# Optimization experiments

Measured on AMD Instinct MI355X. Metric: run time of the kernel, lower is better.

The kernel has to match this reference:

```python
import jax, jax.numpy as jnp
import numpy as np

N = 100000        # nodes
E = 1600000       # edges (avg degree 16)
IN, HID, OUT = 128, 128, 40
K = 3             # Chebyshev order
NUM_HID = 5       # hidden ChebConv layers between first and last


def setup_inputs() -> dict:
    key = jax.random.key(0)
    ks = jax.random.split(key, 8)
    s = 0.05
    return dict(
        features=jax.random.normal(ks[0], (N, IN), jnp.float32),
        src=jax.random.randint(ks[1], (E,), 0, N),
        dst=jax.random.randint(ks[2], (E,), 0, N),
        W0=jax.random.normal(ks[3], (K * IN, HID), jnp.float32) * s,
        b0=jnp.zeros((HID,), jnp.float32),
        Wh=jax.random.normal(ks[4], (NUM_HID, K * HID, HID), jnp.float32) * s,
        bh=jnp.zeros((NUM_HID, HID), jnp.float32),
        Wl=jax.random.normal(ks[5], (K * HID, OUT), jnp.float32) * s,
        bl=jnp.zeros((OUT,), jnp.float32),
    )


def _cheb_conv(X, src, dst, dinv, W, b):
    """One DGL ChebConv with lambda_max=2 (re_norm=1): relu(cat(X_0..X_{K-1}) @ W + b)."""
    def spmm(Y):  # A_hat @ Y = D^-1/2 A D^-1/2 Y via gather/segment-sum
        msg = (Y * dinv)[src]                                  # [E, d]
        return jax.ops.segment_sum(msg, dst, num_segments=N) * dinv

    X0 = X
    bases = [X0]
    X1 = -spmm(X0)                       # X_1 = -A_hat X  (re_norm - 1 == 0)
    bases.append(X1)
    for _ in range(2, K):
        X2 = -2.0 * spmm(X1) - X0        # X_t = -2 A_hat X_{t-1} - X_{t-2}
        bases.append(X2)
        X0, X1 = X1, X2
    Xt = jnp.concatenate(bases, axis=1)  # [N, K*d]
    return jax.nn.relu(Xt @ W + b)


def reference(features, src, dst, W0, b0, Wh, bh, Wl, bl):
    # symmetric normalization from in-degrees (clamped at 1), as in DGL ChebConv
    deg = jax.ops.segment_sum(jnp.ones((E,), jnp.float32), dst, num_segments=N)
    dinv = jnp.clip(deg, 1.0, None) ** -0.5
    dinv = dinv[:, None]                 # [N, 1]

    h = _cheb_conv(features, src, dst, dinv, W0, b0)
    for i in range(NUM_HID):             # dropout is identity in eval mode
        h = _cheb_conv(h, src, dst, dinv, Wh[i], bh[i])
    return _cheb_conv(h, src, dst, dinv, Wl, bl)
```

## Files before the change

kernel.cpp:

```cpp
#include <hip/hip_runtime.h>
#include <hip/hip_bf16.h>


#define NN 100000
#define EE 1600000
#define FF 128
#define NBK 1563
#define EPB 4096
#define CAP 3072
#define QTH1 25000
#define QTH2 50000
#define QTH3 75000

typedef __attribute__((ext_vector_type(8))) short short8_t;
typedef __attribute__((ext_vector_type(8))) _Float16 half8_t;
typedef __attribute__((ext_vector_type(4))) _Float16 half4_t;
typedef __attribute__((ext_vector_type(4))) float floatx4;
typedef __attribute__((ext_vector_type(4))) float accfrag;


__global__ __launch_bounds__(256) void bhist_kernel(const int* __restrict__ dst,
                                                    int* __restrict__ bcnt) {
    __shared__ int lh[NBK];
    int tid = threadIdx.x;
    for (int j = tid; j < NBK; j += 256) lh[j] = 0;
    __syncthreads();
    int e0 = blockIdx.x * EPB;
#pragma unroll
    for (int k = 0; k < EPB / 256; ++k) {
        int i = e0 + k * 256 + tid;
        if (i < EE) atomicAdd(&lh[dst[i] >> 6], 1);
    }
    __syncthreads();
    for (int j = tid; j < NBK; j += 256)
        if (lh[j] > 0) atomicAdd(&bcnt[j], lh[j]);
}

__global__ __launch_bounds__(256) void scan_p1_kernel(const int* __restrict__ cnt,
                                                      int* __restrict__ bsum, int n) {
    __shared__ int red[8];
    int i = blockIdx.x * 256 + threadIdx.x;
    int v = (i < n) ? cnt[i] : 0;
    for (int off = 32; off > 0; off >>= 1) v += __shfl_down(v, off, 64);
    int wv = threadIdx.x >> 6;
    if ((threadIdx.x & 63) == 0) red[wv] = v;
    __syncthreads();
    if (threadIdx.x == 0) bsum[blockIdx.x] = red[0] + red[1] + red[2] + red[3];
}

__global__ __launch_bounds__(1024) void scan_p2_kernel(int* __restrict__ bsum, int nb) {
    __shared__ int s[1024];
    int tid = threadIdx.x;
    int v = (tid < nb) ? bsum[tid] : 0;
    s[tid] = v;
    __syncthreads();
    for (int off = 1; off < 1024; off <<= 1) {
        int u = (tid >= off) ? s[tid - off] : 0;
        __syncthreads();
        s[tid] += u;
        __syncthreads();
    }
    if (tid < nb) bsum[tid] = s[tid] - v;
}

__global__ __launch_bounds__(256) void scan_p3_kernel(const int* __restrict__ cnt,
                                                      const int* __restrict__ bsum,
                                                      int* __restrict__ out_ptr, int n) {
    __shared__ int s[256];
    int tid = threadIdx.x;
    int i = blockIdx.x * 256 + tid;
    int v = (i < n) ? cnt[i] : 0;
    s[tid] = v;
    __syncthreads();
    for (int off = 1; off < 256; off <<= 1) {
        int u = (tid >= off) ? s[tid - off] : 0;
        __syncthreads();
        s[tid] += u;
        __syncthreads();
    }
    if (i < n) {
        int excl = bsum[blockIdx.x] + s[tid] - v;
        out_ptr[i] = excl;
        if (i == n - 1) out_ptr[n] = excl + v;
    }
}

__global__ __launch_bounds__(256) void bscatter_kernel(
    const int* __restrict__ src, const int* __restrict__ dst,
    const int* __restrict__ bptr, int* __restrict__ bfill, int* __restrict__ ebuf) {
    __shared__ int lh[NBK];
    __shared__ int lbase[NBK];
    int tid = threadIdx.x;
    for (int j = tid; j < NBK; j += 256) lh[j] = 0;
    __syncthreads();
    int e0 = blockIdx.x * EPB;
#pragma unroll
    for (int k = 0; k < EPB / 256; ++k) {
        int i = e0 + k * 256 + tid;
        if (i < EE) atomicAdd(&lh[dst[i] >> 6], 1);
    }
    __syncthreads();
    for (int j = tid; j < NBK; j += 256)
        if (lh[j] > 0) lbase[j] = atomicAdd(&bfill[j], lh[j]);
    __syncthreads();
    for (int j = tid; j < NBK; j += 256) lh[j] = 0;
    __syncthreads();
#pragma unroll
    for (int k = 0; k < EPB / 256; ++k) {
        int i = e0 + k * 256 + tid;
        if (i < EE) {
            int d = dst[i];
            int b = d >> 6;
            int off = atomicAdd(&lh[b], 1);
            ebuf[bptr[b] + lbase[b] + off] = (src[i] << 6) | (d & 63);
        }
    }
}

__global__ __launch_bounds__(256) void csr_build_kernel(
    const int* __restrict__ ebuf, const int* __restrict__ bptr,
    int* __restrict__ rowptr, int* __restrict__ colsrc,
    float* __restrict__ dinv, float* __restrict__ dinv2, float* __restrict__ sdeg) {
    __shared__ int pk[CAP];
    __shared__ int ob[CAP];
    __shared__ int cnt[256];
    __shared__ int sexcl[256];
    __shared__ int fill[256];

    int tid = threadIdx.x;
    int b = blockIdx.x;
    int start = bptr[b];
    int cb = bptr[b + 1] - start;
    if (cb > CAP) cb = CAP;

    cnt[tid] = 0; fill[tid] = 0;
    __syncthreads();

    for (int i = tid; i < cb; i += 256) {
        int v = ebuf[start + i];
        pk[i] = v;
        int srcn = v >> 6;
        int qt = (srcn >= QTH3) ? 3 : (srcn >= QTH2) ? 2 : (srcn >= QTH1) ? 1 : 0;
        atomicAdd(&cnt[((v & 63) << 2) | qt], 1);
    }
    __syncthreads();

    if (tid < 64) {
        int base = tid << 2;
        int c0 = cnt[base], c1 = cnt[base + 1], c2 = cnt[base + 2], c3 = cnt[base + 3];
        int lsum = c0 + c1 + c2 + c3;
        int inc = lsum;
        for (int off = 1; off < 64; off <<= 1) {
            int u = __shfl_up(inc, off, 64);
            if (tid >= off) inc += u;
        }
        int lex = inc - lsum;
        sexcl[base]     = lex;
        sexcl[base + 1] = lex + c0;
        sexcl[base + 2] = lex + c0 + c1;
        sexcl[base + 3] = lex + c0 + c1 + c2;
        int gnode = b * 64 + tid;
        if (gnode < NN) {
            rowptr[gnode] = start + lex;
            int d = lsum < 1 ? 1 : lsum;
            float fd = (float)d;
            dinv[gnode]  = 1.0f / sqrtf(fd);
            dinv2[gnode] = 1.0f / fd;
            sdeg[gnode]  = sqrtf(fd);
        }
    }
    if (b == 0 && tid == 0) rowptr[NN] = EE;
    __syncthreads();

    for (int i = tid; i < cb; i += 256) {
        int v = pk[i];
        int srcn = v >> 6;
        int qt = (srcn >= QTH3) ? 3 : (srcn >= QTH2) ? 2 : (srcn >= QTH1) ? 1 : 0;
        int bin = ((v & 63) << 2) | qt;
        int off = atomicAdd(&fill[bin], 1);
        ob[sexcl[bin] + off] = srcn;
    }
    __syncthreads();

    for (int i = tid; i < cb; i += 256) colsrc[start + i] = ob[i];
}


__global__ __launch_bounds__(256) void wprep_kernel(
    const float* __restrict__ W0, const float* __restrict__ Wh, const float* __restrict__ Wl,
    _Float16* __restrict__ Wh16)
{
    int idx = blockIdx.x * 256 + threadIdx.x;
    const int PER = 128 * 384;
    if (idx >= 7 * PER) return;
    int layer = idx / PER;
    int rem = idx - layer * PER;
    int ncol = rem / 384;
    int k = rem - ncol * 384;
    const float* W; int outc;
    if (layer == 0)      { W = W0; outc = 128; }
    else if (layer < 6)  { W = Wh + (size_t)(layer - 1) * 384 * 128; outc = 128; }
    else                 { W = Wl; outc = 40; }
    float v = 0.f;
    if (ncol < outc) {
        v = W[(size_t)k * outc + ncol];
        if (k < 128) v -= W[(size_t)(k + 256) * outc + ncol];
    }
    Wh16[idx] = (_Float16)v;
}


__global__ __launch_bounds__(256) void fcvt_kernel(const float* __restrict__ in,
                                                   const float* __restrict__ dinv,
                                                   _Float16* __restrict__ out, int total4) {
    int i = blockIdx.x * 256 + threadIdx.x;
    if (i >= total4) return;
    int node = i >> 5;
    float dv = dinv[node];
    floatx4 v = *(const floatx4*)&in[i * 4];
    half4_t r = { (_Float16)(dv * v.x), (_Float16)(dv * v.y),
                  (_Float16)(dv * v.z), (_Float16)(dv * v.w) };
    *(half4_t*)&out[i * 4] = r;
}


__global__ __launch_bounds__(256) void spmm_h_kernel(
    _Float16* __restrict__ out, const _Float16* __restrict__ Xin,
    const float* __restrict__ dinv2,
    const int* __restrict__ rp, const int* __restrict__ cs,
    float alpha, int n)
{
    int half = blockIdx.x & 1;
    int nb   = blockIdx.x >> 1;
    int slot = threadIdx.x >> 3;
    int lane = threadIdx.x & 7;
    int node = nb * 32 + slot;
    if (node >= n) return;
    int c8 = half * 8 + lane;
    const half8_t* X8 = (const half8_t*)Xin;
    float acc[8] = { 0.f, 0.f, 0.f, 0.f, 0.f, 0.f, 0.f, 0.f };
    int s = rp[node], e = rp[node + 1];
    int cnt = e - s;
    int efull = s + (cnt & ~7);
    int i = s;
    for (; i < efull; i += 8) {
        int idx[8];
#pragma unroll
        for (int u = 0; u < 8; ++u) idx[u] = cs[i + u];
        half8_t x[8];
#pragma unroll
        for (int u = 0; u < 8; ++u) x[u] = X8[(size_t)idx[u] * 16 + c8];
#pragma unroll
        for (int u = 0; u < 8; ++u)
#pragma unroll
            for (int j = 0; j < 8; ++j) acc[j] += (float)x[u][j];
    }
    if (i < e) {
        int idx[8];
#pragma unroll
        for (int u = 0; u < 8; ++u) {
            int ii = i + u;
            idx[u] = cs[(ii < e) ? ii : (e - 1)];
        }
        half8_t x[8];
#pragma unroll
        for (int u = 0; u < 8; ++u) x[u] = X8[(size_t)idx[u] * 16 + c8];
#pragma unroll
        for (int u = 0; u < 8; ++u) {
            float m = (i + u < e) ? 1.0f : 0.0f;
#pragma unroll
            for (int j = 0; j < 8; ++j) acc[j] = fmaf(m, (float)x[u][j], acc[j]);
        }
    }
    float sc = alpha * dinv2[node];
    half8_t r;
#pragma unroll
    for (int j = 0; j < 8; ++j) r[j] = (_Float16)(sc * acc[j]);
    ((half8_t*)out)[(size_t)node * 16 + c8] = r;
}


template <int OUTC, int NT, bool HOUT>
__global__ __launch_bounds__(256, 4) void gemm_f16_kernel(
    void* __restrict__ outp, const _Float16* __restrict__ X0,
    const _Float16* __restrict__ X1, const _Float16* __restrict__ X2,
    const _Float16* __restrict__ Wh16, const float* __restrict__ bias,
    const float* __restrict__ sdeg, const float* __restrict__ dinv, int n)
{
    __shared__ _Float16 Ws[NT * 16][136];

    int tid = threadIdx.x;
    int lane = tid & 63;
    int wave = tid >> 6;
    int m15 = lane & 15;
    int quad = lane >> 4;
    int row0 = blockIdx.x * 128 + wave * 32;

    accfrag acc[2][NT];
#pragma unroll
    for (int mi = 0; mi < 2; ++mi)
#pragma unroll
        for (int nj = 0; nj < NT; ++nj) acc[mi][nj] = (accfrag){0.f, 0.f, 0.f, 0.f};

    int r0 = row0 + m15;
    int r1 = r0 + 16;
    size_t ro0 = (size_t)((r0 < n) ? r0 : 0) * 16;
    size_t ro1 = (size_t)((r1 < n) ? r1 : 0) * 16;

    const _Float16* srcs[3] = { X0, X1, X2 };

    for (int sb = 0; sb < 3; ++sb) {
        {
            const int VEC = NT * 256;
#pragma unroll
            for (int v0 = 0; v0 < VEC; v0 += 256) {
                int v = v0 + tid;
                int row = v >> 4;
                int c8 = (v & 15) * 8;
                *(half8_t*)&Ws[row][c8] =
                    *(const half8_t*)(Wh16 + (size_t)row * 384 + sb * 128 + c8);
            }
        }
        __syncthreads();

        const half8_t* Xp8 = (const half8_t*)srcs[sb];
#pragma unroll
        for (int kk = 0; kk < 4; ++kk) {
            int k0 = kk * 32 + quad * 8;
            half8_t a0 = Xp8[ro0 + kk * 4 + quad];
            half8_t a1 = Xp8[ro1 + kk * 4 + quad];
#pragma unroll
            for (int nj = 0; nj < NT; ++nj) {
                half8_t bfr = *(const half8_t*)&Ws[nj * 16 + m15][k0];
                acc[0][nj] = __builtin_amdgcn_mfma_f32_16x16x32_f16(a0, bfr, acc[0][nj], 0, 0, 0);
                acc[1][nj] = __builtin_amdgcn_mfma_f32_16x16x32_f16(a1, bfr, acc[1][nj], 0, 0, 0);
            }
        }
        __syncthreads();
    }

    float rs[2][4];
#pragma unroll
    for (int mi = 0; mi < 2; ++mi)
#pragma unroll
        for (int reg = 0; reg < 4; ++reg) {
            int gr = row0 + mi * 16 + quad * 4 + reg;
            int cg = (gr < n) ? gr : 0;
            rs[mi][reg] = HOUT ? dinv[cg] : sdeg[cg];
        }
#pragma unroll
    for (int nj = 0; nj < NT; ++nj) {
        int col = nj * 16 + m15;
        float bv = (col < OUTC) ? bias[col] : 0.f;
#pragma unroll
        for (int mi = 0; mi < 2; ++mi) {
#pragma unroll
            for (int reg = 0; reg < 4; ++reg) {
                int gr = row0 + mi * 16 + quad * 4 + reg;
                if (gr < n && col < OUTC) {
                    if (HOUT) {
                        float v = acc[mi][nj][reg] + rs[mi][reg] * bv;
                        v = v > 0.f ? v : 0.f;
                        ((_Float16*)outp)[(size_t)gr * OUTC + col] = (_Float16)v;
                    } else {
                        float v = rs[mi][reg] * acc[mi][nj][reg] + bv;
                        v = v > 0.f ? v : 0.f;
                        ((float*)outp)[(size_t)gr * OUTC + col] = v;
                    }
                }
            }
        }
    }
}


extern "C" void kernel_launch(void* const* d_in, const int* in_sizes, int n_in,
                              void* d_out, int out_size, void* d_ws, size_t ws_size,
                              hipStream_t stream) {
    const float* features = (const float*)d_in[0];
    const int*   src      = (const int*)d_in[1];
    const int*   dst      = (const int*)d_in[2];
    const float* W0       = (const float*)d_in[3];
    const float* b0       = (const float*)d_in[4];
    const float* Wh       = (const float*)d_in[5];
    const float* bh       = (const float*)d_in[6];
    const float* Wl       = (const float*)d_in[7];
    const float* bl       = (const float*)d_in[8];
    float* out = (float*)d_out;

    const int N = NN, E = EE;
    const int WTOT = 7 * 128 * 384;
    const int EB = (E + EPB - 1) / EPB;
    const int NB2 = (NBK + 255) / 256;

    char* ws = (char*)d_ws;
    size_t off = 0;
    auto alloc = [&](size_t bytes) -> void* {
        void* p = ws + off;
        off += (bytes + 511) & ~(size_t)511;
        return p;
    };
    int*      bcnt   = (int*)alloc((size_t)NBK * 4);
    int*      bfill  = (int*)alloc((size_t)NBK * 4);
    int*      bptr   = (int*)alloc((size_t)(NBK + 1) * 4);
    int*      bsum   = (int*)alloc((size_t)NB2 * 4);
    int*      rowptr = (int*)alloc((size_t)(N + 1) * 4);
    int*      ebuf   = (int*)alloc((size_t)E * 4);
    int*      colsrc = (int*)alloc((size_t)E * 4);
    float*    dinv   = (float*)alloc((size_t)N * 4);
    float*    dinv2  = (float*)alloc((size_t)N * 4);
    float*    sdeg   = (float*)alloc((size_t)N * 4);
    _Float16* Wh16   = (_Float16*)alloc((size_t)WTOT * 2);
    _Float16* XA     = (_Float16*)alloc((size_t)N * FF * 2);
    _Float16* XB     = (_Float16*)alloc((size_t)N * FF * 2);
    _Float16* B1     = (_Float16*)alloc((size_t)N * FF * 2);
    _Float16* B2     = (_Float16*)alloc((size_t)N * FF * 2);

    hipMemsetAsync(bcnt, 0, (size_t)NBK * 4, stream);
    hipMemsetAsync(bfill, 0, (size_t)NBK * 4, stream);
    bhist_kernel<<<EB, 256, 0, stream>>>(dst, bcnt);
    wprep_kernel<<<(WTOT + 255) / 256, 256, 0, stream>>>(W0, Wh, Wl, Wh16);
    scan_p1_kernel<<<NB2, 256, 0, stream>>>(bcnt, bsum, NBK);
    scan_p2_kernel<<<1, 1024, 0, stream>>>(bsum, NB2);
    scan_p3_kernel<<<NB2, 256, 0, stream>>>(bcnt, bsum, bptr, NBK);
    bscatter_kernel<<<EB, 256, 0, stream>>>(src, dst, bptr, bfill, ebuf);
    csr_build_kernel<<<NBK, 256, 0, stream>>>(ebuf, bptr, rowptr, colsrc, dinv, dinv2, sdeg);
    fcvt_kernel<<<(N * FF / 4 + 255) / 256, 256, 0, stream>>>(features, dinv, XA, N * FF / 4);

    const _Float16* cur = XA;
    _Float16* nxt = XB;
    int spmm_grid = 2 * ((N + 31) / 32);
    int gemm_grid = (N + 127) / 128;

    for (int layer = 0; layer < 7; ++layer) {
        const float* b;
        bool last = (layer == 6);
        if (layer == 0)      { b = b0; }
        else if (layer < 6)  { b = bh + (layer - 1) * 128; }
        else                 { b = bl; }
        const _Float16* wl16 = Wh16 + (size_t)layer * 128 * 384;

        spmm_h_kernel<<<spmm_grid, 256, 0, stream>>>(B1, cur, dinv2, rowptr, colsrc, -1.f, N);
        spmm_h_kernel<<<spmm_grid, 256, 0, stream>>>(B2, B1, dinv2, rowptr, colsrc, -2.f, N);

        if (!last)
            gemm_f16_kernel<128, 8, true><<<gemm_grid, 256, 0, stream>>>(
                (void*)nxt, cur, B1, B2, wl16, b, sdeg, dinv, N);
        else
            gemm_f16_kernel<40, 3, false><<<gemm_grid, 256, 0, stream>>>(
                (void*)out, cur, B1, B2, wl16, b, sdeg, dinv, N);

        if (layer < 6) {
            const _Float16* newcur = nxt;
            nxt = (_Float16*)((nxt == XB) ? XA : XB);
            cur = newcur;
        }
    }
}
```

Baseline: 1.102 ms.

## Fuse all layer SpMM and GEMM stages into one persistent cooperative kernel

Replaces the 21 per-layer kernel launches (two SpMMs and a GEMM for each of 7 layers) with a single cooperative persistent kernel. The kernel loops over virtual blocks in each phase and separates phases with grid-wide syncs. This removes launch gaps and tail idle between stages. The cost is grid.sync overhead, occupancy limited by the shared buffer now sized for 128 rows, and the grid size being hardcoded as 256 CUs times blocks per CU.

```diff
diff --git a/kernel.cpp b/kernel.cpp
--- a/kernel.cpp
+++ b/kernel.cpp
@@ -1,5 +1,8 @@
 #include <hip/hip_runtime.h>
 #include <hip/hip_bf16.h>
+#include <hip/hip_cooperative_groups.h>
+
+namespace cg = cooperative_groups;
 
 
 #define NN 100000
@@ -224,151 +227,189 @@
 }
 
 
-__global__ __launch_bounds__(256) void spmm_h_kernel(
+__device__ __forceinline__ void spmm_phase(
     _Float16* __restrict__ out, const _Float16* __restrict__ Xin,
-    const float* __restrict__ dinv2,
-    const int* __restrict__ rp, const int* __restrict__ cs,
-    float alpha, int n)
+    const float* __restrict__ dinv2, const int* __restrict__ rp,
+    const int* __restrict__ cs, float alpha, int n, int nvb)
 {
-    int half = blockIdx.x & 1;
-    int nb   = blockIdx.x >> 1;
-    int slot = threadIdx.x >> 3;
-    int lane = threadIdx.x & 7;
-    int node = nb * 32 + slot;
-    if (node >= n) return;
-    int c8 = half * 8 + lane;
     const half8_t* X8 = (const half8_t*)Xin;
-    float acc[8] = { 0.f, 0.f, 0.f, 0.f, 0.f, 0.f, 0.f, 0.f };
-    int s = rp[node], e = rp[node + 1];
-    int cnt = e - s;
-    int efull = s + (cnt & ~7);
-    int i = s;
-    for (; i < efull; i += 8) {
-        int idx[8];
-#pragma unroll
-        for (int u = 0; u < 8; ++u) idx[u] = cs[i + u];
-        half8_t x[8];
-#pragma unroll
-        for (int u = 0; u < 8; ++u) x[u] = X8[(size_t)idx[u] * 16 + c8];
-#pragma unroll
-        for (int u = 0; u < 8; ++u)
-#pragma unroll
-            for (int j = 0; j < 8; ++j) acc[j] += (float)x[u][j];
-    }
-    if (i < e) {
-        int idx[8];
-#pragma unroll
-        for (int u = 0; u < 8; ++u) {
-            int ii = i + u;
-            idx[u] = cs[(ii < e) ? ii : (e - 1)];
-        }
-        half8_t x[8];
-#pragma unroll
-        for (int u = 0; u < 8; ++u) x[u] = X8[(size_t)idx[u] * 16 + c8];
-#pragma unroll
-        for (int u = 0; u < 8; ++u) {
-            float m = (i + u < e) ? 1.0f : 0.0f;
-#pragma unroll
-            for (int j = 0; j < 8; ++j) acc[j] = fmaf(m, (float)x[u][j], acc[j]);
-        }
-    }
-    float sc = alpha * dinv2[node];
-    half8_t r;
-#pragma unroll
-    for (int j = 0; j < 8; ++j) r[j] = (_Float16)(sc * acc[j]);
-    ((half8_t*)out)[(size_t)node * 16 + c8] = r;
-}
-
+    for (int vb = blockIdx.x; vb < nvb; vb += gridDim.x) {
+        int half = vb & 1;
+        int nb   = vb >> 1;
+        int slot = threadIdx.x >> 3;
+        int lane = threadIdx.x & 7;
+        int node = nb * 32 + slot;
+        if (node >= n) continue;
+        int c8 = half * 8 + lane;
+        float acc[8] = { 0.f, 0.f, 0.f, 0.f, 0.f, 0.f, 0.f, 0.f };
+        int s = rp[node], e = rp[node + 1];
+        int cnt = e - s;
+        int efull = s + (cnt & ~7);
+        int i = s;
+        for (; i < efull; i += 8) {
+            int idx[8];
+#pragma unroll
+            for (int u = 0; u < 8; ++u) idx[u] = cs[i + u];
+            half8_t x[8];
+#pragma unroll
+            for (int u = 0; u < 8; ++u) x[u] = X8[(size_t)idx[u] * 16 + c8];
+#pragma unroll
+            for (int u = 0; u < 8; ++u)
+#pragma unroll
+                for (int j = 0; j < 8; ++j) acc[j] += (float)x[u][j];
+        }
+        if (i < e) {
+            int idx[8];
+#pragma unroll
+            for (int u = 0; u < 8; ++u) {
+                int ii = i + u;
+                idx[u] = cs[(ii < e) ? ii : (e - 1)];
+            }
+            half8_t x[8];
+#pragma unroll
+            for (int u = 0; u < 8; ++u) x[u] = X8[(size_t)idx[u] * 16 + c8];
+#pragma unroll
+            for (int u = 0; u < 8; ++u) {
+                float m = (i + u < e) ? 1.0f : 0.0f;
+#pragma unroll
+                for (int j = 0; j < 8; ++j) acc[j] = fmaf(m, (float)x[u][j], acc[j]);
+            }
+        }
+        float sc = alpha * dinv2[node];
+        half8_t r;
+#pragma unroll
+        for (int j = 0; j < 8; ++j) r[j] = (_Float16)(sc * acc[j]);
+        ((half8_t*)out)[(size_t)node * 16 + c8] = r;
+    }
+}
 
 template <int OUTC, int NT, bool HOUT>
-__global__ __launch_bounds__(256, 4) void gemm_f16_kernel(
-    void* __restrict__ outp, const _Float16* __restrict__ X0,
-    const _Float16* __restrict__ X1, const _Float16* __restrict__ X2,
-    const _Float16* __restrict__ Wh16, const float* __restrict__ bias,
-    const float* __restrict__ sdeg, const float* __restrict__ dinv, int n)
+__device__ void gemm_phase(
+    _Float16 (*Ws)[136], void* __restrict__ outp,
+    const _Float16* __restrict__ X0, const _Float16* __restrict__ X1,
+    const _Float16* __restrict__ X2, const _Float16* __restrict__ Wh16,
+    const float* __restrict__ bias, const float* __restrict__ sdeg,
+    const float* __restrict__ dinv, int n, int nvb)
 {
-    __shared__ _Float16 Ws[NT * 16][136];
-
     int tid = threadIdx.x;
     int lane = tid & 63;
     int wave = tid >> 6;
     int m15 = lane & 15;
     int quad = lane >> 4;
-    int row0 = blockIdx.x * 128 + wave * 32;
-
-    accfrag acc[2][NT];
-#pragma unroll
-    for (int mi = 0; mi < 2; ++mi)
-#pragma unroll
-        for (int nj = 0; nj < NT; ++nj) acc[mi][nj] = (accfrag){0.f, 0.f, 0.f, 0.f};
-
-    int r0 = row0 + m15;
-    int r1 = r0 + 16;
-    size_t ro0 = (size_t)((r0 < n) ? r0 : 0) * 16;
-    size_t ro1 = (size_t)((r1 < n) ? r1 : 0) * 16;
-
-    const _Float16* srcs[3] = { X0, X1, X2 };
-
-    for (int sb = 0; sb < 3; ++sb) {
-        {
-            const int VEC = NT * 256;
-#pragma unroll
-            for (int v0 = 0; v0 < VEC; v0 += 256) {
-                int v = v0 + tid;
-                int row = v >> 4;
-                int c8 = (v & 15) * 8;
-                *(half8_t*)&Ws[row][c8] =
-                    *(const half8_t*)(Wh16 + (size_t)row * 384 + sb * 128 + c8);
-            }
-        }
-        __syncthreads();
-
-        const half8_t* Xp8 = (const half8_t*)srcs[sb];
-#pragma unroll
-        for (int kk = 0; kk < 4; ++kk) {
-            int k0 = kk * 32 + quad * 8;
-            half8_t a0 = Xp8[ro0 + kk * 4 + quad];
-            half8_t a1 = Xp8[ro1 + kk * 4 + quad];
-#pragma unroll
-            for (int nj = 0; nj < NT; ++nj) {
-                half8_t bfr = *(const half8_t*)&Ws[nj * 16 + m15][k0];
-                acc[0][nj] = __builtin_amdgcn_mfma_f32_16x16x32_f16(a0, bfr, acc[0][nj], 0, 0, 0);
-                acc[1][nj] = __builtin_amdgcn_mfma_f32_16x16x32_f16(a1, bfr, acc[1][nj], 0, 0, 0);
-            }
-        }
-        __syncthreads();
-    }
-
-    float rs[2][4];
-#pragma unroll
-    for (int mi = 0; mi < 2; ++mi)
-#pragma unroll
-        for (int reg = 0; reg < 4; ++reg) {
-            int gr = row0 + mi * 16 + quad * 4 + reg;
-            int cg = (gr < n) ? gr : 0;
-            rs[mi][reg] = HOUT ? dinv[cg] : sdeg[cg];
-        }
-#pragma unroll
-    for (int nj = 0; nj < NT; ++nj) {
-        int col = nj * 16 + m15;
-        float bv = (col < OUTC) ? bias[col] : 0.f;
-#pragma unroll
-        for (int mi = 0; mi < 2; ++mi) {
+
+    for (int vb = blockIdx.x; vb < nvb; vb += gridDim.x) {
+        int row0 = vb * 128 + wave * 32;
+
+        accfrag acc[2][NT];
+#pragma unroll
+        for (int mi = 0; mi < 2; ++mi)
+#pragma unroll
+            for (int nj = 0; nj < NT; ++nj) acc[mi][nj] = (accfrag){0.f, 0.f, 0.f, 0.f};
+
+        int r0 = row0 + m15;
+        int r1 = r0 + 16;
+        size_t ro0 = (size_t)((r0 < n) ? r0 : 0) * 16;
+        size_t ro1 = (size_t)((r1 < n) ? r1 : 0) * 16;
+
+        const _Float16* srcs[3] = { X0, X1, X2 };
+
+        for (int sb = 0; sb < 3; ++sb) {
+            {
+                const int VEC = NT * 256;
+#pragma unroll
+                for (int v0 = 0; v0 < VEC; v0 += 256) {
+                    int v = v0 + tid;
+                    int row = v >> 4;
+                    int c8 = (v & 15) * 8;
+                    *(half8_t*)&Ws[row][c8] =
+                        *(const half8_t*)(Wh16 + (size_t)row * 384 + sb * 128 + c8);
+                }
+            }
+            __syncthreads();
+
+            const half8_t* Xp8 = (const half8_t*)srcs[sb];
+#pragma unroll
+            for (int kk = 0; kk < 4; ++kk) {
+                int k0 = kk * 32 + quad * 8;
+                half8_t a0 = Xp8[ro0 + kk * 4 + quad];
+                half8_t a1 = Xp8[ro1 + kk * 4 + quad];
+#pragma unroll
+                for (int nj = 0; nj < NT; ++nj) {
+                    half8_t bfr = *(const half8_t*)&Ws[nj * 16 + m15][k0];
+                    acc[0][nj] = __builtin_amdgcn_mfma_f32_16x16x32_f16(a0, bfr, acc[0][nj], 0, 0, 0);
+                    acc[1][nj] = __builtin_amdgcn_mfma_f32_16x16x32_f16(a1, bfr, acc[1][nj], 0, 0, 0);
+                }
+            }
+            __syncthreads();
+        }
+
+        float rs[2][4];
+#pragma unroll
+        for (int mi = 0; mi < 2; ++mi)
 #pragma unroll
             for (int reg = 0; reg < 4; ++reg) {
                 int gr = row0 + mi * 16 + quad * 4 + reg;
-                if (gr < n && col < OUTC) {
-                    if (HOUT) {
-                        float v = acc[mi][nj][reg] + rs[mi][reg] * bv;
-                        v = v > 0.f ? v : 0.f;
-                        ((_Float16*)outp)[(size_t)gr * OUTC + col] = (_Float16)v;
-                    } else {
-                        float v = rs[mi][reg] * acc[mi][nj][reg] + bv;
-                        v = v > 0.f ? v : 0.f;
-                        ((float*)outp)[(size_t)gr * OUTC + col] = v;
+                int cg = (gr < n) ? gr : 0;
+                rs[mi][reg] = HOUT ? dinv[cg] : sdeg[cg];
+            }
+#pragma unroll
+        for (int nj = 0; nj < NT; ++nj) {
+            int col = nj * 16 + m15;
+            float bv = (col < OUTC) ? bias[col] : 0.f;
+#pragma unroll
+            for (int mi = 0; mi < 2; ++mi) {
+#pragma unroll
+                for (int reg = 0; reg < 4; ++reg) {
+                    int gr = row0 + mi * 16 + quad * 4 + reg;
+                    if (gr < n && col < OUTC) {
+                        if (HOUT) {
+                            float v = acc[mi][nj][reg] + rs[mi][reg] * bv;
+                            v = v > 0.f ? v : 0.f;
+                            ((_Float16*)outp)[(size_t)gr * OUTC + col] = (_Float16)v;
+                        } else {
+                            float v = rs[mi][reg] * acc[mi][nj][reg] + bv;
+                            v = v > 0.f ? v : 0.f;
+                            ((float*)outp)[(size_t)gr * OUTC + col] = v;
+                        }
                     }
                 }
             }
+        }
+    }
+}
+
+
+__global__ __launch_bounds__(256, 4) void layers_kernel(
+    _Float16* XA, _Float16* XB, _Float16* B1, _Float16* B2,
+    const _Float16* Wh16, const float* b0, const float* bh, const float* bl,
+    const float* dinv2, const float* dinv, const float* sdeg,
+    const int* rp, const int* cs, float* out, int n)
+{
+    __shared__ _Float16 WsBuf[128][136];
+    cg::grid_group grid = cg::this_grid();
+
+    const int nvb_s = 2 * ((n + 31) / 32);
+    const int nvb_g = (n + 127) / 128;
+
+    const _Float16* cur = XA;
+    _Float16* nxt = XB;
+
+    for (int layer = 0; layer < 7; ++layer) {
+        spmm_phase(B1, cur, dinv2, rp, cs, -1.f, n, nvb_s);
+        grid.sync();
+        spmm_phase(B2, B1, dinv2, rp, cs, -2.f, n, nvb_s);
+        grid.sync();
+
+        const _Float16* wl16 = Wh16 + (size_t)layer * 128 * 384;
+        if (layer < 6) {
+            const float* b = (layer == 0) ? b0 : (bh + (size_t)(layer - 1) * 128);
+            gemm_phase<128, 8, true>(WsBuf, (void*)nxt, cur, B1, B2, wl16, b, sdeg, dinv, n, nvb_g);
+            grid.sync();
+            const _Float16* nc = nxt;
+            nxt = (nxt == XB) ? XA : XB;
+            cur = nc;
+        } else {
+            gemm_phase<40, 3, false>(WsBuf, (void*)out, cur, B1, B2, wl16, bl, sdeg, dinv, n, nvb_g);
         }
     }
 }
@@ -427,33 +468,17 @@
     csr_build_kernel<<<NBK, 256, 0, stream>>>(ebuf, bptr, rowptr, colsrc, dinv, dinv2, sdeg);
     fcvt_kernel<<<(N * FF / 4 + 255) / 256, 256, 0, stream>>>(features, dinv, XA, N * FF / 4);
 
-    const _Float16* cur = XA;
-    _Float16* nxt = XB;
-    int spmm_grid = 2 * ((N + 31) / 32);
-    int gemm_grid = (N + 127) / 128;
-
-    for (int layer = 0; layer < 7; ++layer) {
-        const float* b;
-        bool last = (layer == 6);
-        if (layer == 0)      { b = b0; }
-        else if (layer < 6)  { b = bh + (layer - 1) * 128; }
-        else                 { b = bl; }
-        const _Float16* wl16 = Wh16 + (size_t)layer * 128 * 384;
-
-        spmm_h_kernel<<<spmm_grid, 256, 0, stream>>>(B1, cur, dinv2, rowptr, colsrc, -1.f, N);
-        spmm_h_kernel<<<spmm_grid, 256, 0, stream>>>(B2, B1, dinv2, rowptr, colsrc, -2.f, N);
-
-        if (!last)
-            gemm_f16_kernel<128, 8, true><<<gemm_grid, 256, 0, stream>>>(
-                (void*)nxt, cur, B1, B2, wl16, b, sdeg, dinv, N);
-        else
-            gemm_f16_kernel<40, 3, false><<<gemm_grid, 256, 0, stream>>>(
-                (void*)out, cur, B1, B2, wl16, b, sdeg, dinv, N);
-
-        if (layer < 6) {
-            const _Float16* newcur = nxt;
-            nxt = (_Float16*)((nxt == XB) ? XA : XB);
-            cur = newcur;
-        }
-    }
-}
+    int nbpc = 0;
+    hipOccupancyMaxActiveBlocksPerMultiprocessor(&nbpc, layers_kernel, 256, 0);
+    if (nbpc < 1) nbpc = 1;
+    if (nbpc > 8) nbpc = 8;
+    int coopGrid = nbpc * 256;
+
+    int n_arg = N;
+    void* kargs[] = {
+        (void*)&XA, (void*)&XB, (void*)&B1, (void*)&B2, (void*)&Wh16,
+        (void*)&b0, (void*)&bh, (void*)&bl, (void*)&dinv2, (void*)&dinv,
+        (void*)&sdeg, (void*)&rowptr, (void*)&colsrc, (void*)&out, (void*)&n_arg };
+    hipLaunchCooperativeKernel((void*)layers_kernel, dim3(coopGrid), dim3(256),
+                               kargs, 0, stream);
+}
```

Measured after the change: 2.674 ms. 2.43x slower.
